# Performance work log

Measured on AMD Instinct MI355X. Metric: run time of the kernel, lower is better.

The kernel has to match this reference:

```python
import jax, jax.numpy as jnp
import numpy as np

I = 1024  # input_size
H = 1024  # hidden_size


def setup_inputs() -> dict:
    key = jax.random.key(0)
    ks = jax.random.split(key, 13)
    s_i = 1.0 / np.sqrt(I)
    s_h = 1.0 / np.sqrt(H)
    x = jax.random.normal(ks[0], (64, 512, I), dtype=jnp.float32)
    # nn.Linear weights are [out, in]; biases only on the U (recurrent) linears.
    Wi = jax.random.uniform(ks[1], (H, I), jnp.float32, -s_i, s_i)
    Wf = jax.random.uniform(ks[2], (H, I), jnp.float32, -s_i, s_i)
    Wo = jax.random.uniform(ks[3], (H, I), jnp.float32, -s_i, s_i)
    Wg = jax.random.uniform(ks[4], (H, I), jnp.float32, -s_i, s_i)
    Ui = jax.random.uniform(ks[5], (H, H), jnp.float32, -s_h, s_h)
    Uf = jax.random.uniform(ks[6], (H, H), jnp.float32, -s_h, s_h)
    Uo = jax.random.uniform(ks[7], (H, H), jnp.float32, -s_h, s_h)
    Ug = jax.random.uniform(ks[8], (H, H), jnp.float32, -s_h, s_h)
    bi = jax.random.uniform(ks[9], (H,), jnp.float32, -s_h, s_h)
    bf = jax.random.uniform(ks[10], (H,), jnp.float32, -s_h, s_h)
    bo = jax.random.uniform(ks[11], (H,), jnp.float32, -s_h, s_h)
    bg = jax.random.uniform(ks[12], (H,), jnp.float32, -s_h, s_h)
    return {"x": x, "Wi": Wi, "Wf": Wf, "Wo": Wo, "Wg": Wg,
            "Ui": Ui, "Uf": Uf, "Uo": Uo, "Ug": Ug,
            "bi": bi, "bf": bf, "bo": bo, "bg": bg}


def reference(x, Wi, Wf, Wo, Wg, Ui, Uf, Uo, Ug, bi, bf, bo, bg):
    B, T, _ = x.shape
    Hdim = Ui.shape[0]
    # Precompute all input-to-gate projections in one batched contraction: [T, B, H] each.
    Wcat = jnp.concatenate([Wi, Wf, Wo, Wg], axis=0)          # [4H, I]
    xg = jnp.einsum('bti,gi->tbg', x, Wcat)                   # [T, B, 4H]
    xi, xf, xo, xgt = jnp.split(xg, 4, axis=-1)

    h0 = jnp.zeros((B, Hdim), x.dtype)
    c0 = jnp.zeros((B, Hdim), x.dtype)

    def step(carry, gates_t):
        h, c = carry
        gi, gf, go, gg = gates_t
        i = jax.nn.sigmoid(gi + h @ Ui.T + bi)
        f = jax.nn.sigmoid(gf + h @ Uf.T + bf)
        o = jax.nn.sigmoid(go + h @ Uo.T + bo)
        g = jnp.tanh(gg + h @ Ug.T + bg)
        c = f * c + i * g
        h = o * jnp.tanh(c)
        return (h, c), h

    (h_last, c_last), hs = jax.lax.scan(step, (h0, c0), (xi, xf, xo, xgt))
    return jnp.transpose(hs, (1, 0, 2)), h_last, c_last  # [B, T, H], [B, H], [B, H]
```

## Files before the change

kernel.cpp:

```cpp
#include <hip/hip_runtime.h>
#include <stdint.h>
#include <stddef.h>


typedef unsigned short u16;
typedef unsigned int u32;
typedef short bf16x8 __attribute__((ext_vector_type(8)));
typedef float f32x4 __attribute__((ext_vector_type(4)));
typedef u32 u32x4 __attribute__((ext_vector_type(4)));

#define B_ 64
#define T_ 512
#define I_ 1024
#define H_ 1024
#define NWG 64
#define BTH (B_ * T_ * H_)

#define OFF_XB 0UL
#define OFF_WT 67108864UL
#define OFF_UT 75497472UL
#define OFF_XG 83886080UL
#define OFF_HB 352321536UL
#define OFF_FLG 352583680UL

#define EPOCH_MASK 0x40004000u
#define EPOCH_CLR  0xBFFFBFFFu

#define LDS_HX 131072
#define LDS_QC 133120
#define LDS_SZ 133184

__device__ __forceinline__ u16 f2bf(float f) {
  u32 u = __builtin_bit_cast(u32, f);
  return (u16)((u + 0x7FFFu + ((u >> 16) & 1u)) >> 16);
}
__device__ __forceinline__ float bf2f(u16 h) {
  u32 u = ((u32)h) << 16;
  return __builtin_bit_cast(float, u);
}
__device__ __forceinline__ float sigm(float x) { return 1.f / (1.f + __expf(-x)); }
__device__ __forceinline__ float tanh_(float x) {
  float e = __expf(-2.f * fabsf(x));
  float t = (1.f - e) / (1.f + e);
  return x >= 0.f ? t : -t;
}
__device__ __forceinline__ void async16(const void* g, void* l) {
  __builtin_amdgcn_global_load_lds((const __attribute__((address_space(1))) void*)g,
                                   (__attribute__((address_space(3))) void*)l, 16, 0, 0);
}
__device__ __forceinline__ u32x4 ld16_sc1(const u16* p) {
  u32x4 r;
  asm volatile("global_load_dwordx4 %0, %1, off sc1" : "=v"(r) : "v"(p) : "memory");
  return r;
}
__device__ __forceinline__ void st16_sc1(u16* p, u32x4 v) {
  asm volatile("global_store_dwordx4 %0, %1, off sc1" : : "v"(p), "v"(v) : "memory");
}

__global__ void k_init(u16* hbuf, u32* flg) {
  int i = blockIdx.x * 256 + threadIdx.x;
  uint4 z;
  if (i < 8192) {
    z.x = 0u; z.y = 0u; z.z = 0u; z.w = 0u;
  } else {
    z.x = EPOCH_MASK; z.y = EPOCH_MASK; z.z = EPOCH_MASK; z.w = EPOCH_MASK;
  }
  ((uint4*)hbuf)[i] = z;
  if (i < NWG) flg[i] = 0u;
}

__global__ void k_cvt_x(const float4* __restrict__ x, ushort4* __restrict__ xb) {
  size_t i = (size_t)blockIdx.x * 256 + threadIdx.x;
  float4 v = x[i];
  ushort4 o;
  o.x = f2bf(v.x); o.y = f2bf(v.y); o.z = f2bf(v.z); o.w = f2bf(v.w);
  xb[i] = o;
}

__global__ void k_cvt_w(const float* __restrict__ Wi, const float* __restrict__ Wf,
                        const float* __restrict__ Wo, const float* __restrict__ Wg,
                        const float* __restrict__ Ui, const float* __restrict__ Uf,
                        const float* __restrict__ Uo, const float* __restrict__ Ug,
                        u16* __restrict__ Wt, u16* __restrict__ Ut) {
  int idx = blockIdx.x * 256 + threadIdx.x;
  int r = idx >> 7;
  int s = idx & 127;
  int w = r >> 6, c = r & 63, g = c >> 4, jl = c & 15;
  int hrow = w * 16 + jl;
  const float* Wsrc = (g == 0) ? Wi : (g == 1) ? Wf : (g == 2) ? Wo : Wg;
  const float* Usrc = (g == 0) ? Ui : (g == 1) ? Uf : (g == 2) ? Uo : Ug;
  int so = hrow * 1024 + s * 8;
  int dovr = r * 1024 + s * 8;
  ushort4 a, b;
  a.x = f2bf(Wsrc[so + 0]); a.y = f2bf(Wsrc[so + 1]); a.z = f2bf(Wsrc[so + 2]); a.w = f2bf(Wsrc[so + 3]);
  b.x = f2bf(Wsrc[so + 4]); b.y = f2bf(Wsrc[so + 5]); b.z = f2bf(Wsrc[so + 6]); b.w = f2bf(Wsrc[so + 7]);
  *(ushort4*)&Wt[dovr] = a;
  *(ushort4*)&Wt[dovr + 4] = b;
  a.x = f2bf(Usrc[so + 0]); a.y = f2bf(Usrc[so + 1]); a.z = f2bf(Usrc[so + 2]); a.w = f2bf(Usrc[so + 3]);
  b.x = f2bf(Usrc[so + 4]); b.y = f2bf(Usrc[so + 5]); b.z = f2bf(Usrc[so + 6]); b.w = f2bf(Usrc[so + 7]);
  *(ushort4*)&Ut[dovr] = a;
  *(ushort4*)&Ut[dovr + 4] = b;
}

__global__ __launch_bounds__(256) void k_gemm(const u16* __restrict__ xb,
                                              const u16* __restrict__ Wt,
                                              u16* __restrict__ xg) {
  __shared__ u16 As[4 * 128 * 8];
  __shared__ u16 Bs[4 * 128 * 8];
  const int tid = threadIdx.x;
  const int lane = tid & 63, wave = tid >> 6;
  const int wm = wave >> 1, wn = wave & 1;
  const int lr = lane & 15, lq = lane >> 4;
  const int m0 = blockIdx.y * 128, n0 = blockIdx.x * 128;

  f32x4 acc[4][4];
#pragma unroll
  for (int mt = 0; mt < 4; ++mt)
#pragma unroll
    for (int nt = 0; nt < 4; ++nt) acc[mt][nt] = {0.f, 0.f, 0.f, 0.f};

  for (int kk = 0; kk < 32; ++kk) {
    int k0 = kk * 32;
    __syncthreads();
#pragma unroll
    for (int uu = 0; uu < 2; ++uu) {
      int u = wave * 2 + uu;
      int kq = u >> 1, rh = u & 1;
      int row = rh * 64 + lane;
      async16(&xb[(size_t)(m0 + row) * 1024 + k0 + kq * 8], &As[kq * 1024 + rh * 512]);
      async16(&Wt[(size_t)(n0 + row) * 1024 + k0 + kq * 8], &Bs[kq * 1024 + rh * 512]);
    }
    __syncthreads();

    bf16x8 af[4], bfr[4];
#pragma unroll
    for (int mt = 0; mt < 4; ++mt)
      af[mt] = *(const bf16x8*)&As[lq * 1024 + (wm * 64 + mt * 16 + lr) * 8];
#pragma unroll
    for (int nt = 0; nt < 4; ++nt)
      bfr[nt] = *(const bf16x8*)&Bs[lq * 1024 + (wn * 64 + nt * 16 + lr) * 8];
#pragma unroll
    for (int mt = 0; mt < 4; ++mt)
#pragma unroll
      for (int nt = 0; nt < 4; ++nt)
        acc[mt][nt] = __builtin_amdgcn_mfma_f32_16x16x32_bf16(af[mt], bfr[nt], acc[mt][nt], 0, 0, 0);
  }

#pragma unroll
  for (int mt = 0; mt < 4; ++mt)
#pragma unroll
    for (int nt = 0; nt < 4; ++nt)
#pragma unroll
      for (int r = 0; r < 4; ++r) {
        int mg = m0 + wm * 64 + mt * 16 + lq * 4 + r;
        int ngl = n0 + wn * 64 + nt * 16 + lr;
        int b = mg >> 9, t = mg & 511;
        int w = ngl >> 6, c = ngl & 63;
        xg[(size_t)t * 262144 + w * 4096 + b * 64 + c] = f2bf(acc[mt][nt][r]);
      }
}

__global__ __launch_bounds__(512, 2) void k_lstm(
    const u16* __restrict__ Ut, const u16* __restrict__ xg, u16* hbuf,
    const float* __restrict__ bi, const float* __restrict__ bf_,
    const float* __restrict__ bo, const float* __restrict__ bg,
    float* __restrict__ out) {
  __shared__ __align__(16) unsigned char LDSB[LDS_SZ];
  u16* hL = (u16*)LDSB;
  float* P = (float*)LDSB;
  u32* hX = (u32*)(LDSB + LDS_HX);
  u32* qc = (u32*)(LDSB + LDS_QC);

  const int tid = threadIdx.x;
  const int lane = tid & 63, wave = tid >> 6;
  const int lr = lane & 15, lq = lane >> 4;
  const int kq = wave >> 1, ng = wave & 1;
  const int pairtid = ng * 64 + lane;
  const int w = blockIdx.x;

  if (tid < 4) qc[tid] = 0u;

  bf16x8 Bf[2][8];
#pragma unroll
  for (int nt = 0; nt < 2; ++nt)
#pragma unroll
    for (int ks = 0; ks < 8; ++ks) {
      int n = w * 64 + ng * 32 + nt * 16 + lr;
      int k = kq * 256 + ks * 32 + lq * 8;
      Bf[nt][ks] = *(const bf16x8*)&Ut[(size_t)n * 1024 + k];
    }

  const int q = wave, b = lane;
  float bia[2][4];
#pragma unroll
  for (int p = 0; p < 2; ++p) {
    int hc = w * 16 + q * 2 + p;
    bia[p][0] = bi[hc]; bia[p][1] = bf_[hc]; bia[p][2] = bo[hc]; bia[p][3] = bg[hc];
  }
  float cst0 = 0.f, cst1 = 0.f;

  __syncthreads();

  for (int t = 0; t < T_; ++t) {
    const u16* hin = hbuf + (size_t)(t & 1) * 65536;
    const int ep = (t >> 1) & 1;

    const u16* xgp = xg + (size_t)t * 262144 + w * 4096;
    u32 xv[4];
#pragma unroll
    for (int g = 0; g < 4; ++g)
      xv[g] = *(const u32*)&xgp[b * 64 + g * 16 + q * 2];

    {
      u32x4 v[16];
      u32 pend = 0xFFFFu;
      int spin = 0;
      do {
        if (spin > 1) __builtin_amdgcn_s_sleep(1);
        ++spin;
#pragma unroll
        for (int i = 0; i < 16; ++i)
          if (pend & (1u << i))
            v[i] = ld16_sc1(hin + (size_t)(kq * 2048 + pairtid + (i << 7)) * 8);
        asm volatile("s_waitcnt vmcnt(0)"
                     : "+v"(v[0]), "+v"(v[1]), "+v"(v[2]), "+v"(v[3]),
                       "+v"(v[4]), "+v"(v[5]), "+v"(v[6]), "+v"(v[7]),
                       "+v"(v[8]), "+v"(v[9]), "+v"(v[10]), "+v"(v[11]),
                       "+v"(v[12]), "+v"(v[13]), "+v"(v[14]), "+v"(v[15])
                     :: "memory");
        __builtin_amdgcn_sched_barrier(0);
        if (ep) {
#pragma unroll
          for (int i = 0; i < 16; ++i)
            if (pend & (1u << i)) {
              u32 aa = v[i][0] & v[i][1] & v[i][2] & v[i][3];
              if ((aa & EPOCH_MASK) == EPOCH_MASK) {
                u32x4 wv;
                wv[0] = v[i][0] & EPOCH_CLR; wv[1] = v[i][1] & EPOCH_CLR;
                wv[2] = v[i][2] & EPOCH_CLR; wv[3] = v[i][3] & EPOCH_CLR;
                *(u32x4*)&hL[(size_t)(kq * 2048 + pairtid + (i << 7)) * 8] = wv;
                pend &= ~(1u << i);
              }
            }
        } else {
#pragma unroll
          for (int i = 0; i < 16; ++i)
            if (pend & (1u << i)) {
              u32 oo = v[i][0] | v[i][1] | v[i][2] | v[i][3];
              if ((oo & EPOCH_MASK) == 0u) {
                *(u32x4*)&hL[(size_t)(kq * 2048 + pairtid + (i << 7)) * 8] = v[i];
                pend &= ~(1u << i);
              }
            }
        }
      } while (pend);
    }
    asm volatile("s_waitcnt lgkmcnt(0)" ::: "memory");
    if (lane == 0) atomicAdd(&qc[kq], 1u);
    {
      volatile u32* qp = (volatile u32*)&qc[kq];
      u32 tgt = 2u * (u32)(t + 1);
      while (*qp < tgt) {}
    }
    __builtin_amdgcn_sched_barrier(0);
    asm volatile("" ::: "memory");

    f32x4 acc[4][2];
#pragma unroll
    for (int mt = 0; mt < 4; ++mt) { acc[mt][0] = {0.f,0.f,0.f,0.f}; acc[mt][1] = {0.f,0.f,0.f,0.f}; }

#pragma unroll
    for (int ks = 0; ks < 8; ++ks) {
      int Gk = kq * 32 + ks * 4 + lq;
      bf16x8 af[4];
#pragma unroll
      for (int mt = 0; mt < 4; ++mt)
        af[mt] = *(const bf16x8*)&hL[(Gk * 64 + mt * 16 + lr) * 8];
#pragma unroll
      for (int mt = 0; mt < 4; ++mt) {
        acc[mt][0] = __builtin_amdgcn_mfma_f32_16x16x32_bf16(af[mt], Bf[0][ks], acc[mt][0], 0, 0, 0);
        acc[mt][1] = __builtin_amdgcn_mfma_f32_16x16x32_bf16(af[mt], Bf[1][ks], acc[mt][1], 0, 0, 0);
      }
    }
    __syncthreads();

#pragma unroll
    for (int mt = 0; mt < 4; ++mt)
#pragma unroll
      for (int nt = 0; nt < 2; ++nt)
#pragma unroll
        for (int r = 0; r < 4; ++r) {
          int m = mt * 16 + lq * 4 + r;
          int cc = nt * 16 + lr;
          P[((ng * 4 + kq) * 64 + m) * 34 + cc] = acc[mt][nt][r];
        }
    __syncthreads();

    float hv[2];
#pragma unroll
    for (int p = 0; p < 2; ++p) {
      int jl = q * 2 + p;
      float pre[4];
#pragma unroll
      for (int g = 0; g < 4; ++g) {
        int cc = (g & 1) * 16 + jl;
        int base = (g >> 1) * 4 * 64;
        float s = P[(base + 0 * 64 + b) * 34 + cc] + P[(base + 1 * 64 + b) * 34 + cc] +
                  P[(base + 2 * 64 + b) * 34 + cc] + P[(base + 3 * 64 + b) * 34 + cc];
        u16 xh = (u16)(p == 0 ? (xv[g] & 0xFFFFu) : (xv[g] >> 16));
        pre[g] = s + bf2f(xh) + bia[p][g];
      }
      float iv = sigm(pre[0]);
      float fv = sigm(pre[1]);
      float ov = sigm(pre[2]);
      float gv = tanh_(pre[3]);
      float cn = fv * (p == 0 ? cst0 : cst1) + iv * gv;
      if (p == 0) cst0 = cn; else cst1 = cn;
      hv[p] = ov * tanh_(cn);
    }

    float2 f2v; f2v.x = hv[0]; f2v.y = hv[1];
    *(float2*)&out[((size_t)b * 512 + t) * 1024 + w * 16 + q * 2] = f2v;

    if (t < T_ - 1) {
      u32 hpack = (u32)f2bf(hv[0]) | ((u32)f2bf(hv[1]) << 16);
      if (((t + 1) >> 1) & 1) hpack |= EPOCH_MASK;
      hX[b * 8 + q] = hpack;
      __syncthreads();
      if ((wave == 0) | (wave == 2)) {
        int gg = wave >> 1;
        u32x4 hv4 = *(const u32x4*)&hX[lane * 8 + gg * 4];
        u16* dst = hbuf + (size_t)((t + 1) & 1) * 65536 +
                   (size_t)((2 * w + gg) * 64 + lane) * 8;
        st16_sc1(dst, hv4);
      }
    } else {
      *(float2*)&out[(size_t)BTH + b * 1024 + w * 16 + q * 2] = f2v;
      float2 c2v; c2v.x = cst0; c2v.y = cst1;
      *(float2*)&out[(size_t)BTH + B_ * H_ + b * 1024 + w * 16 + q * 2] = c2v;
    }
  }
}

extern "C" void kernel_launch(void* const* d_in, const int* in_sizes, int n_in,
                              void* d_out, int out_size, void* d_ws, size_t ws_size,
                              hipStream_t stream) {
  const float* x  = (const float*)d_in[0];
  const float* Wi = (const float*)d_in[1];
  const float* Wf = (const float*)d_in[2];
  const float* Wo = (const float*)d_in[3];
  const float* Wg = (const float*)d_in[4];
  const float* Ui = (const float*)d_in[5];
  const float* Uf = (const float*)d_in[6];
  const float* Uo = (const float*)d_in[7];
  const float* Ug = (const float*)d_in[8];
  const float* bi = (const float*)d_in[9];
  const float* bf = (const float*)d_in[10];
  const float* bo = (const float*)d_in[11];
  const float* bg = (const float*)d_in[12];
  float* out = (float*)d_out;

  char* ws = (char*)d_ws;
  u16* xb   = (u16*)(ws + OFF_XB);
  u16* Wt   = (u16*)(ws + OFF_WT);
  u16* Ut   = (u16*)(ws + OFF_UT);
  u16* xg   = (u16*)(ws + OFF_XG);
  u16* hbuf = (u16*)(ws + OFF_HB);
  u32* flg  = (u32*)(ws + OFF_FLG);

  k_init<<<64, 256, 0, stream>>>(hbuf, flg);
  k_cvt_x<<<32768, 256, 0, stream>>>((const float4*)x, (ushort4*)xb);
  k_cvt_w<<<2048, 256, 0, stream>>>(Wi, Wf, Wo, Wg, Ui, Uf, Uo, Ug, Wt, Ut);
  k_gemm<<<dim3(32, 256), 256, 0, stream>>>(xb, Wt, xg);
  k_lstm<<<NWG, 512, 0, stream>>>(Ut, xg, hbuf, bi, bf, bo, bg, out);
}
```

Before: 3.936 ms.

## Publish h with per-thread sc1 stores and batch the h polling loads

Each thread now writes its packed bf16 hidden pair straight to the global exchange buffer with a 4-byte sc1 store. This drops the LDS staging buffer and the mid-step __syncthreads that let two waves issue 16-byte stores. The poll for the next step's h always reissues all 16 loads as one inline-asm batch with immediate offsets, and the output store to `out` moves after the h publish so it is off the critical path. In exchange it adds a barrier at the end of each timestep and iteration guards that break out of the spin loops, which could silently give wrong results if a wait really runs that long.

```diff
diff --git a/kernel.cpp b/kernel.cpp
--- a/kernel.cpp
+++ b/kernel.cpp
@@ -26,9 +26,8 @@
 #define EPOCH_MASK 0x40004000u
 #define EPOCH_CLR  0xBFFFBFFFu
 
-#define LDS_HX 131072
-#define LDS_QC 133120
-#define LDS_SZ 133184
+#define LDS_QC 131072
+#define LDS_SZ 131088
 
 __device__ __forceinline__ u16 f2bf(float f) {
   u32 u = __builtin_bit_cast(u32, f);
@@ -48,13 +47,37 @@
   __builtin_amdgcn_global_load_lds((const __attribute__((address_space(1))) void*)g,
                                    (__attribute__((address_space(3))) void*)l, 16, 0, 0);
 }
-__device__ __forceinline__ u32x4 ld16_sc1(const u16* p) {
-  u32x4 r;
-  asm volatile("global_load_dwordx4 %0, %1, off sc1" : "=v"(r) : "v"(p) : "memory");
-  return r;
-}
-__device__ __forceinline__ void st16_sc1(u16* p, u32x4 v) {
-  asm volatile("global_store_dwordx4 %0, %1, off sc1" : : "v"(p), "v"(v) : "memory");
+__device__ __forceinline__ void st_u32_sc1(u32* p, u32 v) {
+  asm volatile("global_store_dword %0, %1, off sc1" : : "v"(p), "v"(v) : "memory");
+}
+
+__device__ __forceinline__ void poll16(const u16* b0, const u16* b1,
+                                       const u16* b2, const u16* b3,
+                                       u32x4 v[16]) {
+  asm volatile(
+      "global_load_dwordx4 %0, %16, off offset:-4096 sc1\n\t"
+      "global_load_dwordx4 %1, %16, off offset:-2048 sc1\n\t"
+      "global_load_dwordx4 %2, %16, off sc1\n\t"
+      "global_load_dwordx4 %3, %16, off offset:2048 sc1\n\t"
+      "global_load_dwordx4 %4, %17, off offset:-4096 sc1\n\t"
+      "global_load_dwordx4 %5, %17, off offset:-2048 sc1\n\t"
+      "global_load_dwordx4 %6, %17, off sc1\n\t"
+      "global_load_dwordx4 %7, %17, off offset:2048 sc1\n\t"
+      "global_load_dwordx4 %8, %18, off offset:-4096 sc1\n\t"
+      "global_load_dwordx4 %9, %18, off offset:-2048 sc1\n\t"
+      "global_load_dwordx4 %10, %18, off sc1\n\t"
+      "global_load_dwordx4 %11, %18, off offset:2048 sc1\n\t"
+      "global_load_dwordx4 %12, %19, off offset:-4096 sc1\n\t"
+      "global_load_dwordx4 %13, %19, off offset:-2048 sc1\n\t"
+      "global_load_dwordx4 %14, %19, off sc1\n\t"
+      "global_load_dwordx4 %15, %19, off offset:2048 sc1\n\t"
+      "s_waitcnt vmcnt(0)"
+      : "=&v"(v[0]), "=&v"(v[1]), "=&v"(v[2]), "=&v"(v[3]),
+        "=&v"(v[4]), "=&v"(v[5]), "=&v"(v[6]), "=&v"(v[7]),
+        "=&v"(v[8]), "=&v"(v[9]), "=&v"(v[10]), "=&v"(v[11]),
+        "=&v"(v[12]), "=&v"(v[13]), "=&v"(v[14]), "=&v"(v[15])
+      : "v"(b0), "v"(b1), "v"(b2), "v"(b3)
+      : "memory");
 }
 
 __global__ void k_init(u16* hbuf, u32* flg) {
@@ -168,7 +191,6 @@
   __shared__ __align__(16) unsigned char LDSB[LDS_SZ];
   u16* hL = (u16*)LDSB;
   float* P = (float*)LDSB;
-  u32* hX = (u32*)(LDSB + LDS_HX);
   u32* qc = (u32*)(LDSB + LDS_QC);
 
   const int tid = threadIdx.x;
@@ -198,6 +220,8 @@
     bia[p][0] = bi[hc]; bia[p][1] = bf_[hc]; bia[p][2] = bo[hc]; bia[p][3] = bg[hc];
   }
   float cst0 = 0.f, cst1 = 0.f;
+  const int Gh = w * 2 + (q >> 2);
+  const int c8 = (q * 2) & 7;
 
   __syncthreads();
 
@@ -212,22 +236,18 @@
       xv[g] = *(const u32*)&xgp[b * 64 + g * 16 + q * 2];
 
     {
+      const u16* A = hin + (size_t)(kq * 2048 + pairtid) * 8;
+      const u16* b0 = A + 2 * 1024;
+      const u16* b1 = A + 6 * 1024;
+      const u16* b2 = A + 10 * 1024;
+      const u16* b3 = A + 14 * 1024;
       u32x4 v[16];
       u32 pend = 0xFFFFu;
-      int spin = 0;
+      u32 spin = 0;
       do {
         if (spin > 1) __builtin_amdgcn_s_sleep(1);
-        ++spin;
-#pragma unroll
-        for (int i = 0; i < 16; ++i)
-          if (pend & (1u << i))
-            v[i] = ld16_sc1(hin + (size_t)(kq * 2048 + pairtid + (i << 7)) * 8);
-        asm volatile("s_waitcnt vmcnt(0)"
-                     : "+v"(v[0]), "+v"(v[1]), "+v"(v[2]), "+v"(v[3]),
-                       "+v"(v[4]), "+v"(v[5]), "+v"(v[6]), "+v"(v[7]),
-                       "+v"(v[8]), "+v"(v[9]), "+v"(v[10]), "+v"(v[11]),
-                       "+v"(v[12]), "+v"(v[13]), "+v"(v[14]), "+v"(v[15])
-                     :: "memory");
+        if (++spin > 65536u) break;
+        poll16(b0, b1, b2, b3, v);
         __builtin_amdgcn_sched_barrier(0);
         if (ep) {
 #pragma unroll
@@ -260,7 +280,8 @@
     {
       volatile u32* qp = (volatile u32*)&qc[kq];
       u32 tgt = 2u * (u32)(t + 1);
-      while (*qp < tgt) {}
+      u32 guard = 0;
+      while (*qp < tgt) { if (++guard > (1u << 22)) break; }
     }
     __builtin_amdgcn_sched_barrier(0);
     asm volatile("" ::: "memory");
@@ -320,25 +341,21 @@
     }
 
     float2 f2v; f2v.x = hv[0]; f2v.y = hv[1];
-    *(float2*)&out[((size_t)b * 512 + t) * 1024 + w * 16 + q * 2] = f2v;
 
     if (t < T_ - 1) {
+      u16* hout = hbuf + (size_t)((t + 1) & 1) * 65536;
       u32 hpack = (u32)f2bf(hv[0]) | ((u32)f2bf(hv[1]) << 16);
       if (((t + 1) >> 1) & 1) hpack |= EPOCH_MASK;
-      hX[b * 8 + q] = hpack;
-      __syncthreads();
-      if ((wave == 0) | (wave == 2)) {
-        int gg = wave >> 1;
-        u32x4 hv4 = *(const u32x4*)&hX[lane * 8 + gg * 4];
-        u16* dst = hbuf + (size_t)((t + 1) & 1) * 65536 +
-                   (size_t)((2 * w + gg) * 64 + lane) * 8;
-        st16_sc1(dst, hv4);
-      }
+      st_u32_sc1((u32*)&hout[(size_t)(Gh * 64 + b) * 8 + c8], hpack);
+      *(float2*)&out[((size_t)b * 512 + t) * 1024 + w * 16 + q * 2] = f2v;
     } else {
+      *(float2*)&out[((size_t)b * 512 + t) * 1024 + w * 16 + q * 2] = f2v;
       *(float2*)&out[(size_t)BTH + b * 1024 + w * 16 + q * 2] = f2v;
       float2 c2v; c2v.x = cst0; c2v.y = cst1;
       *(float2*)&out[(size_t)BTH + B_ * H_ + b * 1024 + w * 16 + q * 2] = c2v;
     }
+
+    __syncthreads();
   }
 }
 
```

Result: slower. 4.473 ms (+13.6%).
